# Kernel tuning notes

Hardware: AMD Instinct MI355X
Metric: run time of the kernel (lower is better)

Reference implementation:

```python
import jax, jax.numpy as jnp
import numpy as np

D_MODEL = 1024
NHEAD = 16
HEAD_DIM = D_MODEL // NHEAD
FF = 4096
ALPHA = 1.4142135  # deepnorm_alpha
WIN = (127, 128)   # sliding window (left, right)
EPS = 1e-5
ROPE_BASE = 10000.0


def rmsnorm(x, g):
    ms = jnp.mean(x * x, axis=-1, keepdims=True)
    return x * jax.lax.rsqrt(ms + EPS) * g


def rope(x):
    # x: [B, T, H, D]; non-interleaved rotary over full head dim
    T, D = x.shape[1], x.shape[-1]
    half = D // 2
    inv_freq = 1.0 / (ROPE_BASE ** (jnp.arange(half, dtype=jnp.float32) * 2.0 / D))
    ang = jnp.arange(T, dtype=jnp.float32)[:, None] * inv_freq[None, :]  # [T, half]
    cos = jnp.cos(ang)[None, :, None, :]
    sin = jnp.sin(ang)[None, :, None, :]
    x1, x2 = x[..., :half], x[..., half:]
    return jnp.concatenate([x1 * cos - x2 * sin, x2 * cos + x1 * sin], axis=-1)


def setup_inputs() -> dict:
    key = jax.random.key(0)
    ks = jax.random.split(key, 8)
    d, h = D_MODEL, FF
    return {
        "x": jax.random.normal(ks[0], (2, 2048, d), jnp.float32),
        "Wqkv": jax.random.normal(ks[1], (3 * d, d), jnp.float32) * 0.02,
        "Wout": jax.random.normal(ks[2], (d, d), jnp.float32) * 0.02,
        "bout": jnp.zeros((d,), jnp.float32),
        "W1": jax.random.normal(ks[3], (2 * h, d), jnp.float32) * 0.02,
        "W2": jax.random.normal(ks[4], (d, h), jnp.float32) * 0.02,
        "g1": jnp.ones((d,), jnp.float32),
        "g2": jnp.ones((d,), jnp.float32),
    }


def reference(x, Wqkv, Wout, bout, W1, W2, g1, g2):
    B, T, d = x.shape
    # --- self attention with RoPE + sliding window band mask ---
    qkv = (x @ Wqkv.T).reshape(B, T, 3, NHEAD, HEAD_DIM)
    q, k, v = qkv[:, :, 0], qkv[:, :, 1], qkv[:, :, 2]  # [B,T,H,Dh]
    q = rope(q)
    k = rope(k)
    q = jnp.swapaxes(q, 1, 2)  # [B,H,T,Dh]
    k = jnp.swapaxes(k, 1, 2)
    v = jnp.swapaxes(v, 1, 2)
    scale = 1.0 / np.sqrt(HEAD_DIM)
    scores = jnp.einsum('bhqd,bhkd->bhqk', q, k) * scale
    idx = jnp.arange(T)
    rel = idx[None, :] - idx[:, None]  # j - i
    band = (rel >= -WIN[0]) & (rel <= WIN[1])  # [T,T] allowed positions
    scores = jnp.where(band[None, None], scores, -jnp.inf)
    attn = jax.nn.softmax(scores, axis=-1)
    o = jnp.einsum('bhqk,bhkd->bhqd', attn, v)
    o = jnp.swapaxes(o, 1, 2).reshape(B, T, d)
    a = o @ Wout.T + bout
    # --- deepnorm residual 1 + RMSNorm ---
    x1 = a + ALPHA * x
    x2 = rmsnorm(x1, g1)
    # --- SwiGLU MLP: y, gate = fc1(x).chunk(2); y*gate*sigmoid(gate) ---
    yg = x2 @ W1.T
    y, gate = jnp.split(yg, 2, axis=-1)
    y = y * gate * jax.nn.sigmoid(gate)
    y = y @ W2.T
    # --- deepnorm residual 2 + RMSNorm ---
    x3 = y + ALPHA * x2
    return rmsnorm(x3, g2)
```

## Files before the change

kernel.cpp:

```cpp
#include <hip/hip_runtime.h>

#define T_SEQ   2048
#define NHEADS  16
#define DHEAD   64
#define DMODEL  1024
#define ALPHA_C 1.4142135f
#define EPS_C   1e-5f

typedef __attribute__((ext_vector_type(8))) short bf16x8;
typedef __attribute__((ext_vector_type(4))) short bf16x4;
typedef __attribute__((ext_vector_type(4))) float floatx4;

__device__ __forceinline__ float bf2f(unsigned short u) {
  union { unsigned int i; float f; } v;
  v.i = ((unsigned int)u) << 16;
  return v.f;
}
__device__ __forceinline__ unsigned short f2bf(float f) {
  union { float f; unsigned int i; } v;
  v.f = f;
  unsigned int u = v.i;
  u += 0x7FFF + ((u >> 16) & 1);
  return (unsigned short)(u >> 16);
}

__device__ __forceinline__ void gload_lds16(const void* g, void* l) {
  __builtin_amdgcn_global_load_lds(
      (const __attribute__((address_space(1))) void*)g,
      (__attribute__((address_space(3))) void*)l, 16, 0, 0);
}

__global__ void convert_all(const float* __restrict__ Wqkv,
                            const float* __restrict__ Wout,
                            const float* __restrict__ W1,
                            const float* __restrict__ W2,
                            const float* __restrict__ x,
                            unsigned short* __restrict__ ws)
{
  size_t i = ((size_t)blockIdx.x * 256 + threadIdx.x) * 8;
  const float* src;
  size_t off;
  if      (i <  3145728) { src = Wqkv; off = i; }
  else if (i <  4194304) { src = Wout; off = i -  3145728; }
  else if (i < 12582912) { src = W1;   off = i -  4194304; }
  else if (i < 16777216) { src = W2;   off = i - 12582912; }
  else                   { src = x;    off = i - 16777216; }
  floatx4 a = *(const floatx4*)(src + off);
  floatx4 b = *(const floatx4*)(src + off + 4);
  bf16x8 o;
  #pragma unroll
  for (int u = 0; u < 4; u++) {
    o[u]     = (short)f2bf(a[u]);
    o[4 + u] = (short)f2bf(b[u]);
  }
  *(bf16x8*)(ws + i) = o;
}

__global__ void build_rope_lut(float* __restrict__ cosT,
                               float* __restrict__ sinT)
{
  int gid = blockIdx.x * 256 + threadIdx.x;
  int t = gid >> 5, i = gid & 31;
  float fr = powf(10000.f, -(float)i * (1.f / 32.f));
  float sn, cs;
  sincosf((float)t * fr, &sn, &cs);
  cosT[gid] = cs;
  sinT[gid] = sn;
}

template<int BN>
__global__ __launch_bounds__(256) void gemm_lds(
    const unsigned short* __restrict__ A,
    const unsigned short* __restrict__ W,
    unsigned short* __restrict__ C,
    const float* __restrict__ bias,
    int M, int N, int K, int lda)
{
  constexpr int WN = BN / 2;
  constexpr int NJ = WN / 16;
  __shared__ unsigned short As[128 * 32];
  __shared__ unsigned short Bs[BN * 32];

  const int tid  = threadIdx.x;
  const int lane = tid & 63;
  const int wave = tid >> 6;
  const int wm = (wave >> 1) * 64;
  const int wn = (wave & 1) * WN;
  const int mBase = blockIdx.y * 128;
  const int nBase = blockIdx.x * BN;

  const int sRow = lane >> 2;
  const int sCol = (lane & 3) * 8;

  floatx4 acc[4][NJ];
  #pragma unroll
  for (int i = 0; i < 4; i++)
    #pragma unroll
    for (int j = 0; j < NJ; j++) acc[i][j] = (floatx4){0.f, 0.f, 0.f, 0.f};

  const int mrow = lane & 15;
  const int kq   = (lane >> 4) * 8;

  for (int kb = 0; kb < K; kb += 32) {
    __syncthreads();
    #pragma unroll
    for (int j = 0; j < 2; j++) {
      int r = wave * 32 + j * 16 + sRow;
      gload_lds16(A + (size_t)(mBase + r) * lda + kb + sCol,
                  &As[wave * 1024 + j * 512 + lane * 8]);
    }
    if constexpr (BN == 128) {
      #pragma unroll
      for (int j = 0; j < 2; j++) {
        int r = wave * 32 + j * 16 + sRow;
        gload_lds16(W + (size_t)(nBase + r) * K + kb + sCol,
                    &Bs[wave * 1024 + j * 512 + lane * 8]);
      }
    } else {
      int r = wave * 16 + sRow;
      gload_lds16(W + (size_t)(nBase + r) * K + kb + sCol,
                  &Bs[wave * 512 + lane * 8]);
    }
    __syncthreads();

    bf16x8 af[4], bfr[NJ];
    #pragma unroll
    for (int i = 0; i < 4; i++)
      af[i] = *(const bf16x8*)&As[(wm + i * 16 + mrow) * 32 + kq];
    #pragma unroll
    for (int j = 0; j < NJ; j++)
      bfr[j] = *(const bf16x8*)&Bs[(wn + j * 16 + mrow) * 32 + kq];
    #pragma unroll
    for (int i = 0; i < 4; i++)
      #pragma unroll
      for (int j = 0; j < NJ; j++)
        acc[i][j] = __builtin_amdgcn_mfma_f32_16x16x32_bf16(af[i], bfr[j], acc[i][j], 0, 0, 0);
  }

  const int col0 = lane & 15;
  const int row0 = (lane >> 4) * 4;
  #pragma unroll
  for (int j = 0; j < NJ; j++) {
    const int col = nBase + wn + j * 16 + col0;
    const float badd = bias ? bias[col] : 0.f;
    #pragma unroll
    for (int i = 0; i < 4; i++) {
      #pragma unroll
      for (int r = 0; r < 4; r++) {
        const int row = mBase + wm + i * 16 + row0 + r;
        C[(size_t)row * N + col] = f2bf(acc[i][j][r] + badd);
      }
    }
  }
}

__global__ __launch_bounds__(256) void gemm_w2_splitk(
    const unsigned short* __restrict__ A,
    const unsigned short* __restrict__ W,
    float* __restrict__ Cp)
{
  __shared__ unsigned short As[128 * 32];
  __shared__ unsigned short Bs[64 * 32];

  const int tid  = threadIdx.x;
  const int lane = tid & 63;
  const int wave = tid >> 6;
  const int wm = (wave >> 1) * 64;
  const int wn = (wave & 1) * 32;
  const int mBase = blockIdx.y * 128;
  const int nBase = blockIdx.x * 64;
  const int kOff  = blockIdx.z * 2048;

  const int sRow = lane >> 2;
  const int sCol = (lane & 3) * 8;

  floatx4 acc[4][2];
  #pragma unroll
  for (int i = 0; i < 4; i++)
    #pragma unroll
    for (int j = 0; j < 2; j++) acc[i][j] = (floatx4){0.f, 0.f, 0.f, 0.f};

  const int mrow = lane & 15;
  const int kq   = (lane >> 4) * 8;

  for (int kb = 0; kb < 2048; kb += 32) {
    __syncthreads();
    #pragma unroll
    for (int j = 0; j < 2; j++) {
      int r = wave * 32 + j * 16 + sRow;
      gload_lds16(A + (size_t)(mBase + r) * 4096 + kOff + kb + sCol,
                  &As[wave * 1024 + j * 512 + lane * 8]);
    }
    {
      int r = wave * 16 + sRow;
      gload_lds16(W + (size_t)(nBase + r) * 4096 + kOff + kb + sCol,
                  &Bs[wave * 512 + lane * 8]);
    }
    __syncthreads();

    bf16x8 af[4], bfr[2];
    #pragma unroll
    for (int i = 0; i < 4; i++)
      af[i] = *(const bf16x8*)&As[(wm + i * 16 + mrow) * 32 + kq];
    #pragma unroll
    for (int j = 0; j < 2; j++)
      bfr[j] = *(const bf16x8*)&Bs[(wn + j * 16 + mrow) * 32 + kq];
    #pragma unroll
    for (int i = 0; i < 4; i++)
      #pragma unroll
      for (int j = 0; j < 2; j++)
        acc[i][j] = __builtin_amdgcn_mfma_f32_16x16x32_bf16(af[i], bfr[j], acc[i][j], 0, 0, 0);
  }

  const int col0 = lane & 15;
  const int row0 = (lane >> 4) * 4;
  float* dst = Cp + (size_t)blockIdx.z * 4096 * 1024;
  #pragma unroll
  for (int j = 0; j < 2; j++) {
    const int col = nBase + wn + j * 16 + col0;
    #pragma unroll
    for (int i = 0; i < 4; i++)
      #pragma unroll
      for (int r = 0; r < 4; r++) {
        const int row = mBase + wm + i * 16 + row0 + r;
        dst[(size_t)row * 1024 + col] = acc[i][j][r];
      }
  }
}

__global__ __launch_bounds__(256) void gemm_qkv_rope(
    const unsigned short* __restrict__ A,
    const unsigned short* __restrict__ W,
    const float* __restrict__ cosT,
    const float* __restrict__ sinT,
    unsigned short* __restrict__ Qd,
    unsigned short* __restrict__ Kd,
    unsigned short* __restrict__ Vd)
{
  constexpr int K = 1024;
  __shared__ unsigned short As[128 * 32];
  __shared__ unsigned short Bs[128 * 32];

  const int tid  = threadIdx.x;
  const int lane = tid & 63;
  const int wave = tid >> 6;
  const int wm = (wave >> 1) * 64;
  const int wn = (wave & 1) * 64;
  const int mBase = blockIdx.y * 128;
  const int nBase = blockIdx.x * 128;

  const int sRow = lane >> 2;
  const int sCol = (lane & 3) * 8;

  floatx4 acc[4][4];
  #pragma unroll
  for (int i = 0; i < 4; i++)
    #pragma unroll
    for (int j = 0; j < 4; j++) acc[i][j] = (floatx4){0.f, 0.f, 0.f, 0.f};

  const int mrow = lane & 15;
  const int kq   = (lane >> 4) * 8;

  for (int kb = 0; kb < K; kb += 32) {
    __syncthreads();
    #pragma unroll
    for (int j = 0; j < 2; j++) {
      int r = wave * 32 + j * 16 + sRow;
      gload_lds16(A + (size_t)(mBase + r) * K + kb + sCol,
                  &As[wave * 1024 + j * 512 + lane * 8]);
      gload_lds16(W + (size_t)(nBase + r) * K + kb + sCol,
                  &Bs[wave * 1024 + j * 512 + lane * 8]);
    }
    __syncthreads();

    bf16x8 af[4], bfr[4];
    #pragma unroll
    for (int i = 0; i < 4; i++) {
      af[i]  = *(const bf16x8*)&As[(wm + i * 16 + mrow) * 32 + kq];
      bfr[i] = *(const bf16x8*)&Bs[(wn + i * 16 + mrow) * 32 + kq];
    }
    #pragma unroll
    for (int i = 0; i < 4; i++)
      #pragma unroll
      for (int j = 0; j < 4; j++)
        acc[i][j] = __builtin_amdgcn_mfma_f32_16x16x32_bf16(af[i], bfr[j], acc[i][j], 0, 0, 0);
  }

  const int col0 = lane & 15;
  const int row0 = (lane >> 4) * 4;
  const int colBase = nBase + wn;
  const int sect = colBase >> 10;
  const int h    = (colBase & 1023) >> 6;
  unsigned short* dst = (sect == 0) ? Qd : (sect == 1) ? Kd : Vd;

  if (sect < 2) {
    #pragma unroll
    for (int it = 0; it < 4; it++) {
      #pragma unroll
      for (int r = 0; r < 4; r++) {
        const int row = mBase + wm + it * 16 + row0 + r;
        const int b = row >> 11, t = row & 2047;
        size_t ob = ((size_t)((b * NHEADS + h) * T_SEQ + t)) * DHEAD;
        const int tb = t * 32;
        float c0 = cosT[tb + col0],      s0 = sinT[tb + col0];
        float c1 = cosT[tb + col0 + 16], s1 = sinT[tb + col0 + 16];
        float x1a = acc[it][0][r], x2a = acc[it][2][r];
        float x1b = acc[it][1][r], x2b = acc[it][3][r];
        dst[ob + col0]      = f2bf(x1a * c0 - x2a * s0);
        dst[ob + col0 + 32] = f2bf(x2a * c0 + x1a * s0);
        dst[ob + col0 + 16] = f2bf(x1b * c1 - x2b * s1);
        dst[ob + col0 + 48] = f2bf(x2b * c1 + x1b * s1);
      }
    }
  } else {
    #pragma unroll
    for (int it = 0; it < 4; it++)
      #pragma unroll
      for (int j = 0; j < 4; j++)
        #pragma unroll
        for (int r = 0; r < 4; r++) {
          const int row = mBase + wm + it * 16 + row0 + r;
          const int b = row >> 11, t = row & 2047;
          dst[((size_t)((b * NHEADS + h) * T_SEQ + t)) * DHEAD + j * 16 + col0] =
              f2bf(acc[it][j][r]);
        }
  }
}

__global__ __launch_bounds__(256) void gemm_w1_swiglu(
    const unsigned short* __restrict__ A,
    const unsigned short* __restrict__ W1,
    unsigned short* __restrict__ ys)
{
  constexpr int K = 1024;
  __shared__ unsigned short As[128 * 32];
  __shared__ unsigned short Bs[128 * 32];

  const int tid  = threadIdx.x;
  const int lane = tid & 63;
  const int wave = tid >> 6;
  const int wm = (wave >> 1) * 64;
  const int wn = (wave & 1) * 32;
  const int mBase = blockIdx.y * 128;
  const int nBase = blockIdx.x * 64;

  const int sRow = lane >> 2;
  const int sCol = (lane & 3) * 8;

  floatx4 accY[4][2], accG[4][2];
  #pragma unroll
  for (int i = 0; i < 4; i++)
    #pragma unroll
    for (int j = 0; j < 2; j++) {
      accY[i][j] = (floatx4){0.f, 0.f, 0.f, 0.f};
      accG[i][j] = (floatx4){0.f, 0.f, 0.f, 0.f};
    }

  const int mrow = lane & 15;
  const int kq   = (lane >> 4) * 8;
  const int half = wave >> 1;

  for (int kb = 0; kb < K; kb += 32) {
    __syncthreads();
    #pragma unroll
    for (int j = 0; j < 2; j++) {
      int r = wave * 32 + j * 16 + sRow;
      gload_lds16(A + (size_t)(mBase + r) * K + kb + sCol,
                  &As[wave * 1024 + j * 512 + lane * 8]);
    }
    #pragma unroll
    for (int j = 0; j < 2; j++) {
      int r = (wave & 1) * 32 + j * 16 + sRow;
      gload_lds16(W1 + (size_t)(half * 4096 + nBase + r) * K + kb + sCol,
                  &Bs[half * 2048 + (wave & 1) * 1024 + j * 512 + lane * 8]);
    }
    __syncthreads();

    bf16x8 af[4], by[2], bg[2];
    #pragma unroll
    for (int i = 0; i < 4; i++)
      af[i] = *(const bf16x8*)&As[(wm + i * 16 + mrow) * 32 + kq];
    #pragma unroll
    for (int j = 0; j < 2; j++) {
      by[j] = *(const bf16x8*)&Bs[(wn + j * 16 + mrow) * 32 + kq];
      bg[j] = *(const bf16x8*)&Bs[2048 + (wn + j * 16 + mrow) * 32 + kq];
    }
    #pragma unroll
    for (int i = 0; i < 4; i++)
      #pragma unroll
      for (int j = 0; j < 2; j++) {
        accY[i][j] = __builtin_amdgcn_mfma_f32_16x16x32_bf16(af[i], by[j], accY[i][j], 0, 0, 0);
        accG[i][j] = __builtin_amdgcn_mfma_f32_16x16x32_bf16(af[i], bg[j], accG[i][j], 0, 0, 0);
      }
  }

  const int col0 = lane & 15;
  const int row0 = (lane >> 4) * 4;
  #pragma unroll
  for (int j = 0; j < 2; j++) {
    const int col = nBase + wn + j * 16 + col0;
    #pragma unroll
    for (int i = 0; i < 4; i++) {
      #pragma unroll
      for (int r = 0; r < 4; r++) {
        const int row = mBase + wm + i * 16 + row0 + r;
        float y = accY[i][j][r], g = accG[i][j][r];
        float sig = 1.f / (1.f + __expf(-g));
        ys[(size_t)row * 4096 + col] = f2bf(y * g * sig);
      }
    }
  }
}

__global__ __launch_bounds__(256) void attn_mfma(
    const unsigned short* __restrict__ Qg,
    const unsigned short* __restrict__ Kg,
    const unsigned short* __restrict__ Vg,
    unsigned short* __restrict__ Og)
{
  __shared__ unsigned short KV[23040];
  __shared__ unsigned short Qs[64 * 72];
  __shared__ unsigned short Ps[4 * 16 * 328];

  const int tid  = threadIdx.x;
  const int lane = tid & 63;
  const int wave = tid >> 6;
  const int c    = lane & 15;
  const int quad = lane >> 4;
  const int blk  = blockIdx.x;
  const int bh   = blk >> 5;
  const int qBase = (blk & 31) * 64;
  const size_t hbase = (size_t)bh * T_SEQ * DHEAD;

  for (int e = tid; e < 320 * 8; e += 256) {
    int row = e >> 3, ch = e & 7;
    int kg = qBase - 127 + row;
    int kgc = min(max(kg, 0), T_SEQ - 1);
    *(bf16x8*)&KV[row * 72 + ch * 8] =
        *(const bf16x8*)(Kg + hbase + (size_t)kgc * DHEAD + ch * 8);
  }
  for (int e = tid; e < 64 * 8; e += 256) {
    int row = e >> 3, ch = e & 7;
    *(bf16x8*)&Qs[row * 72 + ch * 8] =
        *(const bf16x8*)(Qg + hbase + (size_t)(qBase + row) * DHEAD + ch * 8);
  }
  __syncthreads();

  bf16x8 aq[2];
  #pragma unroll
  for (int hh = 0; hh < 2; hh++)
    aq[hh] = *(const bf16x8*)&Qs[(wave * 16 + c) * 72 + hh * 32 + quad * 8];

  floatx4 s[20];
  #pragma unroll
  for (int kt = 0; kt < 20; kt++) {
    bf16x8 b0 = *(const bf16x8*)&KV[(kt * 16 + c) * 72 + quad * 8];
    bf16x8 b1 = *(const bf16x8*)&KV[(kt * 16 + c) * 72 + 32 + quad * 8];
    floatx4 t = (floatx4){0.f, 0.f, 0.f, 0.f};
    t = __builtin_amdgcn_mfma_f32_16x16x32_bf16(aq[0], b0, t, 0, 0, 0);
    t = __builtin_amdgcn_mfma_f32_16x16x32_bf16(aq[1], b1, t, 0, 0, 0);
    s[kt] = t;
  }
  __syncthreads();

  for (int ch = wave; ch < 5; ch += 4) {
    int koff = ch * 64 + lane;
    int kg = qBase - 127 + koff;
    int kgc = min(max(kg, 0), T_SEQ - 1);
    const unsigned short* vrow = Vg + hbase + (size_t)kgc * DHEAD;
    #pragma unroll
    for (int dg = 0; dg < 8; dg++) {
      bf16x8 v8 = *(const bf16x8*)(vrow + dg * 8);
      #pragma unroll
      for (int j = 0; j < 8; j++)
        KV[(dg * 8 + j) * 328 + koff] = (unsigned short)v8[j];
    }
  }

  const int kLoMin = max(0, 127 - qBase);
  const int kHiMax = min(319, 2047 + 127 - qBase);
  float mx[4] = {-3e38f, -3e38f, -3e38f, -3e38f};
  #pragma unroll
  for (int kt = 0; kt < 20; kt++) {
    const int koff = kt * 16 + c;
    #pragma unroll
    for (int reg = 0; reg < 4; reg++) {
      const int qrow = wave * 16 + quad * 4 + reg;
      const int d = koff - qrow;
      bool ok = (d >= 0) && (d <= 255) && (koff >= kLoMin) && (koff <= kHiMax);
      float val = ok ? s[kt][reg] * 0.125f : -3e38f;
      s[kt][reg] = val;
      mx[reg] = fmaxf(mx[reg], val);
    }
  }
  #pragma unroll
  for (int reg = 0; reg < 4; reg++)
    #pragma unroll
    for (int m = 1; m <= 8; m <<= 1)
      mx[reg] = fmaxf(mx[reg], __shfl_xor(mx[reg], m));

  float ls[4] = {0.f, 0.f, 0.f, 0.f};
  #pragma unroll
  for (int kt = 0; kt < 20; kt++) {
    const int koff = kt * 16 + c;
    #pragma unroll
    for (int reg = 0; reg < 4; reg++) {
      float p = __expf(s[kt][reg] - mx[reg]);
      ls[reg] += p;
      Ps[wave * 5248 + (quad * 4 + reg) * 328 + koff] = f2bf(p);
    }
  }
  float inv[4];
  #pragma unroll
  for (int reg = 0; reg < 4; reg++) {
    #pragma unroll
    for (int m = 1; m <= 8; m <<= 1) ls[reg] += __shfl_xor(ls[reg], m);
    inv[reg] = 1.f / ls[reg];
  }
  __syncthreads();

  floatx4 oacc[4];
  #pragma unroll
  for (int nt = 0; nt < 4; nt++) oacc[nt] = (floatx4){0.f, 0.f, 0.f, 0.f};
  #pragma unroll
  for (int kt2 = 0; kt2 < 10; kt2++) {
    bf16x8 a = *(const bf16x8*)&Ps[wave * 5248 + c * 328 + kt2 * 32 + quad * 8];
    #pragma unroll
    for (int nt = 0; nt < 4; nt++) {
      bf16x8 bb = *(const bf16x8*)&KV[(nt * 16 + c) * 328 + kt2 * 32 + quad * 8];
      oacc[nt] = __builtin_amdgcn_mfma_f32_16x16x32_bf16(a, bb, oacc[nt], 0, 0, 0);
    }
  }

  const int b = bh >> 4, h = bh & 15;
  #pragma unroll
  for (int nt = 0; nt < 4; nt++) {
    #pragma unroll
    for (int reg = 0; reg < 4; reg++) {
      const int qg = qBase + wave * 16 + quad * 4 + reg;
      Og[((size_t)(b * T_SEQ + qg)) * DMODEL + h * DHEAD + nt * 16 + c] =
          f2bf(oacc[nt][reg] * inv[reg]);
    }
  }
}

__global__ __launch_bounds__(256) void rmsnorm_mid(
    const unsigned short* __restrict__ a,
    const float* __restrict__ x,
    const float* __restrict__ g,
    unsigned short* __restrict__ out)
{
  __shared__ float red[4];
  const int row = blockIdx.x;
  const int tid = threadIdx.x;
  const size_t base = (size_t)row * DMODEL;
  const int c = tid * 4;
  bf16x4  av = *(const bf16x4*)(a + base + c);
  floatx4 xv = *(const floatx4*)(x + base + c);
  floatx4 gv = *(const floatx4*)(g + c);
  float s[4], ss = 0.f;
  #pragma unroll
  for (int j = 0; j < 4; j++) {
    s[j] = bf2f((unsigned short)av[j]) + ALPHA_C * xv[j];
    ss += s[j] * s[j];
  }
  #pragma unroll
  for (int m = 1; m <= 32; m <<= 1) ss += __shfl_xor(ss, m);
  if ((tid & 63) == 0) red[tid >> 6] = ss;
  __syncthreads();
  float ms = (red[0] + red[1] + red[2] + red[3]) * (1.f / DMODEL);
  float scl = rsqrtf(ms + EPS_C);
  bf16x4 ov;
  #pragma unroll
  for (int j = 0; j < 4; j++) ov[j] = (short)f2bf(s[j] * scl * gv[j]);
  *(bf16x4*)(out + base + c) = ov;
}

__global__ __launch_bounds__(256) void rmsnorm_final_sk(
    const float* __restrict__ p0,
    const float* __restrict__ p1,
    const unsigned short* __restrict__ x2,
    const float* __restrict__ g,
    float* __restrict__ out)
{
  __shared__ float red[4];
  const int row = blockIdx.x;
  const int tid = threadIdx.x;
  const size_t base = (size_t)row * DMODEL;
  const int c = tid * 4;
  floatx4 a0 = *(const floatx4*)(p0 + base + c);
  floatx4 a1 = *(const floatx4*)(p1 + base + c);
  bf16x4  xv = *(const bf16x4*)(x2 + base + c);
  floatx4 gv = *(const floatx4*)(g + c);
  float s[4], ss = 0.f;
  #pragma unroll
  for (int j = 0; j < 4; j++) {
    s[j] = (a0[j] + a1[j]) + ALPHA_C * bf2f((unsigned short)xv[j]);
    ss += s[j] * s[j];
  }
  #pragma unroll
  for (int m = 1; m <= 32; m <<= 1) ss += __shfl_xor(ss, m);
  if ((tid & 63) == 0) red[tid >> 6] = ss;
  __syncthreads();
  float ms = (red[0] + red[1] + red[2] + red[3]) * (1.f / DMODEL);
  float scl = rsqrtf(ms + EPS_C);
  floatx4 ov;
  #pragma unroll
  for (int j = 0; j < 4; j++) ov[j] = s[j] * scl * gv[j];
  *(floatx4*)(out + base + c) = ov;
}

extern "C" void kernel_launch(void* const* d_in, const int* in_sizes, int n_in,
                              void* d_out, int out_size, void* d_ws, size_t ws_size,
                              hipStream_t stream) {
  (void)in_sizes; (void)n_in; (void)out_size; (void)ws_size;
  const float* x    = (const float*)d_in[0];
  const float* Wqkv = (const float*)d_in[1];
  const float* Wout = (const float*)d_in[2];
  const float* bout = (const float*)d_in[3];
  const float* W1   = (const float*)d_in[4];
  const float* W2   = (const float*)d_in[5];
  const float* g1   = (const float*)d_in[6];
  const float* g2   = (const float*)d_in[7];
  float* out = (float*)d_out;

  unsigned short* ws    = (unsigned short*)d_ws;
  unsigned short* Wqkvb = ws;
  unsigned short* Woutb = ws + 3145728;
  unsigned short* W1b   = ws + 4194304;
  unsigned short* W2b   = ws + 12582912;
  unsigned short* P1    = ws + 16777216;
  unsigned short* x2    = ws + 20971520;
  unsigned short* q     = ws + 25165824;
  unsigned short* k     = ws + 29360128;
  unsigned short* v     = ws + 33554432;
  unsigned short* o     = ws + 37748736;
  unsigned short* ys    = ws + 25165824;
  float* cosT = (float*)(ws + 37748736);
  float* sinT = cosT + 65536;
  float* p0   = (float*)(ws + 41943040);
  float* p1   = (float*)(ws + 50331648);

  build_rope_lut<<<256, 256, 0, stream>>>(cosT, sinT);
  convert_all<<<10240, 256, 0, stream>>>(Wqkv, Wout, W1, W2, x, ws);
  gemm_qkv_rope<<<dim3(24, 32), 256, 0, stream>>>(P1, Wqkvb, cosT, sinT, q, k, v);
  attn_mfma<<<32 * (T_SEQ / 64), 256, 0, stream>>>(q, k, v, o);
  gemm_lds<64><<<dim3(16, 32), 256, 0, stream>>>(o, Woutb, P1, bout, 4096, 1024, 1024, 1024);
  rmsnorm_mid<<<4096, 256, 0, stream>>>(P1, x, g1, x2);
  gemm_w1_swiglu<<<dim3(64, 32), 256, 0, stream>>>(x2, W1b, ys);
  gemm_w2_splitk<<<dim3(16, 32, 2), 256, 0, stream>>>(ys, W2b, p0);
  rmsnorm_final_sk<<<4096, 256, 0, stream>>>(p0, p1, x2, g2, out);
}
```

Measured before the change: 401.5 us.

## Rewrite W1 SwiGLU GEMM as 256x256 tile, 8-wave, phased double-buffered pipeline

Replaces the 128x64 single-buffered W1+SwiGLU GEMM with a 512-thread kernel that computes 256 rows by 128 output columns (256 W1 rows, y and gate together) using K-tiles of 64. Loads into LDS are double-buffered and interleaved across four MFMA phases, with XOR-swizzled LDS addressing, s_setprio around MFMA bursts and a block-index remap for L2 locality. The aim is to hide global-load latency and raise MFMA density and operand reuse. In exchange it uses 128KB of LDS and many accumulators per thread, which limits occupancy, and it depends on hand-placed waitcnt and barrier ordering being correct.

```diff
diff --git a/kernel.cpp b/kernel.cpp
--- a/kernel.cpp
+++ b/kernel.cpp
@@ -327,89 +327,151 @@
   }
 }
 
-__global__ __launch_bounds__(256) void gemm_w1_swiglu(
+#define BAR() __builtin_amdgcn_s_barrier()
+#define LGKM0() do { asm volatile("s_waitcnt lgkmcnt(0)" ::: "memory"); \
+                     __builtin_amdgcn_sched_barrier(0); } while (0)
+
+#define RD_A(bb, mh)                                                      \
+  _Pragma("unroll") for (int i = 0; i < 4; i++)                           \
+  _Pragma("unroll") for (int s = 0; s < 2; s++)                           \
+    af[i][s] = *(const bf16x8*)&lds[(bb) + aRd +                          \
+        ((mh) * 64 + i * 16 + mrow) * 64 + s * 32 + kqu];
+
+#define RD_B(bb, nh)                                                      \
+  _Pragma("unroll") for (int n = 0; n < 2; n++)                           \
+  _Pragma("unroll") for (int s = 0; s < 2; s++)                           \
+    bf[(nh) * 2 + n][s] = *(const bf16x8*)&lds[(bb) + bRd +               \
+        (bRow0 + ((nh) * 2 + n) * 16 + mrow) * 64 + s * 32 + kqu];
+
+#define MFMA16(mh, nh)                                                    \
+  _Pragma("unroll") for (int i = 0; i < 4; i++)                           \
+  _Pragma("unroll") for (int n = 0; n < 2; n++)                           \
+  _Pragma("unroll") for (int s = 0; s < 2; s++)                           \
+    acc[(mh) * 4 + i][(nh) * 2 + n] =                                     \
+        __builtin_amdgcn_mfma_f32_16x16x32_bf16(                          \
+            af[i][s], bf[(nh) * 2 + n][s],                                \
+            acc[(mh) * 4 + i][(nh) * 2 + n], 0, 0, 0);
+
+__global__ __launch_bounds__(512, 2) void gemm_w1_swiglu_8ph(
     const unsigned short* __restrict__ A,
     const unsigned short* __restrict__ W1,
     unsigned short* __restrict__ ys)
 {
-  constexpr int K = 1024;
-  __shared__ unsigned short As[128 * 32];
-  __shared__ unsigned short Bs[128 * 32];
+  __shared__ unsigned short lds[65536];
 
   const int tid  = threadIdx.x;
   const int lane = tid & 63;
-  const int wave = tid >> 6;
-  const int wm = (wave >> 1) * 64;
-  const int wn = (wave & 1) * 32;
-  const int mBase = blockIdx.y * 128;
-  const int nBase = blockIdx.x * 64;
-
-  const int sRow = lane >> 2;
-  const int sCol = (lane & 3) * 8;
-
-  floatx4 accY[4][2], accG[4][2];
-  #pragma unroll
-  for (int i = 0; i < 4; i++)
-    #pragma unroll
-    for (int j = 0; j < 2; j++) {
-      accY[i][j] = (floatx4){0.f, 0.f, 0.f, 0.f};
-      accG[i][j] = (floatx4){0.f, 0.f, 0.f, 0.f};
-    }
-
+  const int wid  = tid >> 6;
+  const int wr   = wid >> 2;
+  const int wc   = wid & 3;
   const int mrow = lane & 15;
-  const int kq   = (lane >> 4) * 8;
-  const int half = wave >> 1;
-
-  for (int kb = 0; kb < K; kb += 32) {
-    __syncthreads();
-    #pragma unroll
-    for (int j = 0; j < 2; j++) {
-      int r = wave * 32 + j * 16 + sRow;
-      gload_lds16(A + (size_t)(mBase + r) * K + kb + sCol,
-                  &As[wave * 1024 + j * 512 + lane * 8]);
-    }
-    #pragma unroll
-    for (int j = 0; j < 2; j++) {
-      int r = (wave & 1) * 32 + j * 16 + sRow;
-      gload_lds16(W1 + (size_t)(half * 4096 + nBase + r) * K + kb + sCol,
-                  &Bs[half * 2048 + (wave & 1) * 1024 + j * 512 + lane * 8]);
-    }
-    __syncthreads();
-
-    bf16x8 af[4], by[2], bg[2];
-    #pragma unroll
-    for (int i = 0; i < 4; i++)
-      af[i] = *(const bf16x8*)&As[(wm + i * 16 + mrow) * 32 + kq];
-    #pragma unroll
-    for (int j = 0; j < 2; j++) {
-      by[j] = *(const bf16x8*)&Bs[(wn + j * 16 + mrow) * 32 + kq];
-      bg[j] = *(const bf16x8*)&Bs[2048 + (wn + j * 16 + mrow) * 32 + kq];
-    }
-    #pragma unroll
-    for (int i = 0; i < 4; i++)
-      #pragma unroll
-      for (int j = 0; j < 2; j++) {
-        accY[i][j] = __builtin_amdgcn_mfma_f32_16x16x32_bf16(af[i], by[j], accY[i][j], 0, 0, 0);
-        accG[i][j] = __builtin_amdgcn_mfma_f32_16x16x32_bf16(af[i], bg[j], accG[i][j], 0, 0, 0);
-      }
+  const int kqu  = ((lane >> 4) * 8) ^ ((mrow & 4) ? 16 : 0);
+
+  const int bid   = blockIdx.y * 32 + blockIdx.x;
+  const int nb    = (bid & 7) * 64 + (bid >> 3);
+  const int mBase = (nb >> 5) * 256;
+  const int nBase = (nb & 31) * 128;
+
+  const int r0 = tid >> 3;
+  const int ce = (((tid * 16) & 127) >> 1) ^ ((r0 & 4) ? 16 : 0);
+  const size_t aoff0 = (size_t)(mBase + r0) * 1024 + ce;
+  const size_t aoff1 = aoff0 + (size_t)64 * 1024;
+  auto growf = [&](int br) {
+    int col = nBase + (br >> 6) * 32 + (br & 31);
+    return ((br >> 5) & 1) ? 4096 + col : col;
+  };
+  const size_t boff00 = (size_t)growf(r0)       * 1024 + ce;
+  const size_t boff01 = (size_t)growf(64 + r0)  * 1024 + ce;
+  const size_t boff10 = (size_t)growf(128 + r0) * 1024 + ce;
+  const size_t boff11 = (size_t)growf(192 + r0) * 1024 + ce;
+  const int d0 = tid * 8;
+
+  auto stA = [&](int buf, int h, int kt) {
+    const unsigned short* g = A + (size_t)kt * 64 + (h ? (size_t)128 * 1024 : 0);
+    int base = buf * 32768 + h * 8192;
+    gload_lds16(g + aoff0, &lds[base + d0]);
+    gload_lds16(g + aoff1, &lds[base + 4096 + d0]);
+  };
+  auto stB = [&](int buf, int h, int kt) {
+    const unsigned short* g = W1 + (size_t)kt * 64;
+    int base = buf * 32768 + 16384 + h * 8192;
+    gload_lds16(g + (h ? boff10 : boff00), &lds[base + d0]);
+    gload_lds16(g + (h ? boff11 : boff01), &lds[base + 4096 + d0]);
+  };
+
+  floatx4 acc[8][4];
+  #pragma unroll
+  for (int i = 0; i < 8; i++)
+    #pragma unroll
+    for (int n = 0; n < 4; n++) acc[i][n] = (floatx4){0.f, 0.f, 0.f, 0.f};
+  bf16x8 af[4][2], bf[4][2];
+
+  const int aRd   = wr * 8192;
+  const int bRd   = 16384 + (wc >> 1) * 8192;
+  const int bRow0 = (wc & 1) * 64;
+
+  stB(0, 0, 0); stA(0, 0, 0); stA(0, 1, 0); stB(0, 1, 0);
+  stB(1, 0, 1); stA(1, 0, 1);
+  asm volatile("s_waitcnt vmcnt(4)" ::: "memory");
+  BAR();
+
+  for (int t = 0; t < 16; ++t) {
+    const int cur = t & 1;
+    const int nxt = cur ^ 1;
+    const int bb  = cur * 32768;
+    const int ta  = (t + 1 < 16) ? t + 1 : 15;
+    const int tb  = (t + 2 < 16) ? t + 2 : 15;
+
+    RD_A(bb, 0); RD_B(bb, 0);
+    stA(nxt, 1, ta);
+    BAR(); LGKM0();
+    __builtin_amdgcn_s_setprio(1);
+    MFMA16(0, 0);
+    __builtin_amdgcn_s_setprio(0);
+    BAR();
+
+    RD_B(bb, 1);
+    stB(nxt, 1, ta);
+    BAR(); LGKM0();
+    __builtin_amdgcn_s_setprio(1);
+    MFMA16(0, 1);
+    __builtin_amdgcn_s_setprio(0);
+    BAR();
+
+    RD_A(bb, 1);
+    stB(cur, 0, tb);
+    BAR(); LGKM0();
+    __builtin_amdgcn_s_setprio(1);
+    MFMA16(1, 1);
+    __builtin_amdgcn_s_setprio(0);
+    BAR();
+
+    stA(cur, 0, tb);
+    BAR(); LGKM0();
+    __builtin_amdgcn_s_setprio(1);
+    MFMA16(1, 0);
+    __builtin_amdgcn_s_setprio(0);
+    asm volatile("s_waitcnt vmcnt(4)" ::: "memory");
+    BAR();
   }
 
   const int col0 = lane & 15;
   const int row0 = (lane >> 4) * 4;
   #pragma unroll
-  for (int j = 0; j < 2; j++) {
-    const int col = nBase + wn + j * 16 + col0;
-    #pragma unroll
-    for (int i = 0; i < 4; i++) {
+  for (int n = 0; n < 2; n++) {
+    const int col = nBase + wc * 32 + n * 16 + col0;
+    #pragma unroll
+    for (int i = 0; i < 8; i++) {
+      const int rowb = mBase + wr * 128 + i * 16 + row0;
       #pragma unroll
       for (int r = 0; r < 4; r++) {
-        const int row = mBase + wm + i * 16 + row0 + r;
-        float y = accY[i][j][r], g = accG[i][j][r];
+        float y = acc[i][n][r], g = acc[i][n + 2][r];
         float sig = 1.f / (1.f + __expf(-g));
-        ys[(size_t)row * 4096 + col] = f2bf(y * g * sig);
+        ys[(size_t)(rowb + r) * 4096 + col] = f2bf(y * g * sig);
       }
     }
   }
+  asm volatile("s_waitcnt vmcnt(0)" ::: "memory");
 }
 
 __global__ __launch_bounds__(256) void attn_mfma(
@@ -647,7 +709,7 @@
   attn_mfma<<<32 * (T_SEQ / 64), 256, 0, stream>>>(q, k, v, o);
   gemm_lds<64><<<dim3(16, 32), 256, 0, stream>>>(o, Woutb, P1, bout, 4096, 1024, 1024, 1024);
   rmsnorm_mid<<<4096, 256, 0, stream>>>(P1, x, g1, x2);
-  gemm_w1_swiglu<<<dim3(64, 32), 256, 0, stream>>>(x2, W1b, ys);
+  gemm_w1_swiglu_8ph<<<dim3(32, 16), 512, 0, stream>>>(x2, W1b, ys);
   gemm_w2_splitk<<<dim3(16, 32, 2), 256, 0, stream>>>(ys, W2b, p0);
   rmsnorm_final_sk<<<4096, 256, 0, stream>>>(p0, p1, x2, g2, out);
 }
```

After: 394.1 us. No clear change (-1.9%).
